# Kernel optimization log

Measured on AMD Instinct MI355X. Metric: run time of the kernel, lower is better.

The kernel has to match this reference:

```python
import jax, jax.numpy as jnp
import numpy as np

T, H, W = 64, 1024, 1024
GRAD_PCT = 0.15
BZ_PCT = 0.3      # 30th percentile of |Bz|


def setup_inputs() -> dict:
    key = jax.random.key(0)
    k1, k2, k3 = jax.random.split(key, 3)
    frames = jax.random.normal(k1, (T, H, W), dtype=jnp.float32)
    observed_mask = jnp.ones((T,), dtype=bool)
    conv_w = jax.random.normal(k2, (4, 1, 3), dtype=jnp.float32) * 0.3  # depthwise OIH
    conv_b = jax.random.normal(k3, (4,), dtype=jnp.float32) * 0.1
    return {"frames": frames, "observed_mask": observed_mask,
            "conv_w": conv_w, "conv_b": conv_b}


def _pil_stats(frames):
    # frames: [T,H,W] -> stats [T,4] (length, intensity, x_centroid, y_centroid)
    T_, H_, W_ = frames.shape
    N = H_ * W_
    gx = jnp.pad(frames[:, :, 1:] - frames[:, :, :-1], ((0, 0), (0, 0), (0, 1)))
    gy = jnp.pad(frames[:, 1:, :] - frames[:, :-1, :], ((0, 0), (0, 1), (0, 0)))
    gm = jnp.sqrt(gx * gx + gy * gy)                    # [T,H,W]
    gm_flat = gm.reshape(T_, N)
    thr = jnp.sort(gm_flat, axis=-1)[:, int((1.0 - GRAD_PCT) * (N - 1))]
    bz_abs = jnp.abs(frames).reshape(T_, N)
    bz_thr = jnp.sort(bz_abs, axis=-1)[:, int(BZ_PCT * (N - 1))]
    mask = ((gm_flat > thr[:, None]) & (bz_abs < bz_thr[:, None])).astype(frames.dtype)
    pil_sum = jnp.clip(mask.sum(-1), 1e-6)
    length = pil_sum / N
    intensity = (gm_flat * mask).sum(-1) / pil_sum
    w3 = (mask * gm_flat).reshape(T_, H_, W_)           # centroid weights
    wsum = jnp.clip(w3.sum((1, 2)), 1e-6)
    xs = jnp.arange(W_, dtype=frames.dtype)
    ys = jnp.arange(H_, dtype=frames.dtype)
    x_cent = jnp.einsum('thw,w->t', w3, xs) / wsum / W_
    y_cent = jnp.einsum('thw,h->t', w3, ys) / wsum / H_
    return jnp.stack([length, intensity, x_cent, y_cent], axis=-1)


def reference(frames, observed_mask, conv_w, conv_b):
    # observed_mask is all-True -> all T frames observed (static n_obs = T)
    n = frames.shape[0]
    stats = _pil_stats(frames)                          # [T,4]
    x = stats.T[None]                                   # [1,4,T]
    y = jax.lax.conv_general_dilated(
        x, conv_w, window_strides=(1,), padding=((1, 1),),
        feature_group_count=4, dimension_numbers=('NCH', 'OIH', 'NCH'))
    s = (y + conv_b[None, :, None])[0].T                # [T,4] smoothed
    length, intensity, x_cent, y_cent = s[:, 0], s[:, 1], s[:, 2], s[:, 3]
    length_mean = length.mean()
    intensity_mean = intensity.mean()
    t_norm = jnp.linspace(0.0, 1.0, n)
    length_trend = ((length - length_mean) * (t_norm - 0.5)).sum() * 6 / n
    intensity_trend = ((intensity - intensity_mean) * (t_norm - 0.5)).sum() * 6 / n
    dx = x_cent[1:] - x_cent[:-1]
    dy = y_cent[1:] - y_cent[:-1]
    speeds = jnp.sqrt(dx * dx + dy * dy)
    motion_speed = speeds.mean()
    motion_direction = jnp.arctan2(dy.sum(), dx.sum()) / np.pi
    growth_rate = (length[-1] - length[0]) / max(1, n - 1)
    instability = jnp.std(speeds, ddof=1)               # unbiased, per-step speeds
    return jnp.stack([length_mean, length_trend, intensity_mean, intensity_trend,
                      motion_speed, motion_direction, growth_rate, instability])
```

## Files before the change

### kernel.cpp

```cpp
#include <hip/hip_runtime.h>
#include <math.h>
#include <stddef.h>

constexpr int T_ = 64;
constexpr int H_ = 1024;
constexpr int W_ = 1024;
constexpr int N_ = H_ * W_;
constexpr unsigned RANK_G = 891288;
constexpr unsigned RANK_B = 314572;

constexpr int ROWS_PER_BLOCK = 32;
constexpr int BLOCKS_PER_FRAME = H_ / ROWS_PER_BLOCK;

constexpr int SROWS = 16;
constexpr int NS = SROWS * W_;
constexpr int SHB = 8192;
constexpr int MARGIN = 192;
constexpr int RS_G = (int)(RANK_G / 64);
constexpr int RS_B = (int)(RANK_B / 64);

constexpr unsigned CAPG = 1536;
constexpr unsigned CAPB = 1536;
constexpr unsigned CAPX = 448;

constexpr unsigned CACHE_N = 26624;
constexpr int SEL_THREADS = 512;

constexpr int RES_SPLIT = 8;

typedef float f4_t __attribute__((ext_vector_type(4)));

struct WS {
  unsigned lo[2][T_], hi[2][T_];
  unsigned cntG[T_][32], cntB[T_][32], cntX[T_][32];
  unsigned cbG[T_][32], cbB[T_][32];
  float    thr[2][T_];
  double   part[T_][32][4];
  double   acc2[T_][RES_SPLIT][4];
  unsigned Gg[T_][32][CAPG];
  unsigned Ga[T_][32][CAPG];
  unsigned Bb[T_][32][CAPB];
  unsigned Xg[T_][32][CAPX];
  unsigned Xb[T_][32][CAPX];
  unsigned Xa[T_][32][CAPX];
};

__device__ __forceinline__ float gm_at(float cur, float right, float down,
                                       int col, int row) {
  float gx = (col < W_ - 1) ? (right - cur) : 0.0f;
  float gy = (row < H_ - 1) ? (down - cur) : 0.0f;
  return sqrtf(gx * gx + gy * gy);
}

template <int NT>
__device__ __forceinline__ unsigned excl_scan_block(unsigned v, int tx,
                                                    volatile unsigned* wsum) {
  const int lane = tx & 63, wv = tx >> 6;
  unsigned s = v;
#pragma unroll
  for (int o = 1; o < 64; o <<= 1) {
    unsigned u = __shfl_up(s, o);
    if (lane >= o) s += u;
  }
  if (lane == 63) wsum[wv] = s;
  __syncthreads();
  unsigned base = 0;
#pragma unroll
  for (int w = 0; w < NT / 64; ++w)
    if (w < wv) base += wsum[w];
  __syncthreads();
  return base + s - v;
}

__global__ __launch_bounds__(256) void sample_kernel(const float* __restrict__ frames,
                                                     WS* ws) {
  const int t = blockIdx.x;
  __shared__ unsigned hist[2][SHB];
  __shared__ unsigned sub[4][1024];
  __shared__ unsigned wscan[4];
  __shared__ unsigned selB[4], selCB[4];
  const int tx = threadIdx.x, c = tx * 4, lane = tx & 63;
  for (int i = tx; i < 2 * SHB; i += 256) (&hist[0][0])[i] = 0;
  for (int i = tx; i < 4 * 1024; i += 256) (&sub[0][0])[i] = 0;
  __syncthreads();
  const float* f = frames + (size_t)t * N_;

#pragma unroll 4
  for (int r = 0; r < SROWS; ++r) {
    const int h = r * 64 + 32;
    const float* row = f + (size_t)h * W_;
    f4_t a = *(const f4_t*)(row + c);
    f4_t b = *(const f4_t*)(row + W_ + c);
    float an = __shfl_down(a.x, 1);
    if (lane == 63) an = (c + 4 < W_) ? row[c + 4] : 0.0f;
    float xs[5] = {a.x, a.y, a.z, a.w, an};
    float ys[4] = {b.x, b.y, b.z, b.w};
#pragma unroll
    for (int j = 0; j < 4; ++j) {
      float gm = gm_at(xs[j], xs[j + 1], ys[j], c + j, h);
      float bz = fabsf(xs[j]);
      atomicAdd(&hist[0][__float_as_uint(gm) >> 18], 1u);
      atomicAdd(&hist[1][__float_as_uint(bz) >> 18], 1u);
    }
  }
  __syncthreads();

  for (int q = 0; q < 2; ++q) {
    unsigned s = 0;
#pragma unroll
    for (int j = 0; j < SHB / 256; ++j) s += hist[q][tx * (SHB / 256) + j];
    unsigned cb = excl_scan_block<256>(s, tx, wscan);
#pragma unroll
    for (int e = 0; e < 2; ++e) {
      int k = (q == 0 ? RS_G : RS_B) + (e == 0 ? -MARGIN : MARGIN);
      if ((unsigned)k >= cb && (unsigned)k < cb + s) {
        unsigned rem = (unsigned)k - cb, cum = 0;
        for (int j = 0; j < SHB / 256; ++j) {
          unsigned hv = hist[q][tx * (SHB / 256) + j];
          if (rem < cum + hv) {
            selB[q * 2 + e]  = tx * (SHB / 256) + j;
            selCB[q * 2 + e] = cb + cum;
            break;
          }
          cum += hv;
        }
      }
    }
    __syncthreads();
  }

#pragma unroll 4
  for (int r = 0; r < SROWS; ++r) {
    const int h = r * 64 + 32;
    const float* row = f + (size_t)h * W_;
    f4_t a = *(const f4_t*)(row + c);
    f4_t b = *(const f4_t*)(row + W_ + c);
    float an = __shfl_down(a.x, 1);
    if (lane == 63) an = (c + 4 < W_) ? row[c + 4] : 0.0f;
    float xs[5] = {a.x, a.y, a.z, a.w, an};
    float ys[4] = {b.x, b.y, b.z, b.w};
#pragma unroll
    for (int j = 0; j < 4; ++j) {
      float gm = gm_at(xs[j], xs[j + 1], ys[j], c + j, h);
      float bz = fabsf(xs[j]);
      unsigned ug = __float_as_uint(gm), ub = __float_as_uint(bz);
#pragma unroll
      for (int e = 0; e < 2; ++e) {
        if ((ug >> 18) == selB[e])     atomicAdd(&sub[e][(ug >> 8) & 1023u], 1u);
        if ((ub >> 18) == selB[2 + e]) atomicAdd(&sub[2 + e][(ub >> 8) & 1023u], 1u);
      }
    }
  }
  __syncthreads();

  for (int qe = 0; qe < 4; ++qe) {
    unsigned s = 0;
#pragma unroll
    for (int j = 0; j < 4; ++j) s += sub[qe][tx * 4 + j];
    unsigned cb = excl_scan_block<256>(s, tx, wscan);
    int q = qe >> 1, e = qe & 1;
    int k0 = (q == 0 ? RS_G : RS_B) + (e == 0 ? -MARGIN : MARGIN);
    unsigned k = (unsigned)k0 - selCB[qe];
    if (k >= cb && k < cb + s) {
      unsigned rem = k - cb, cum = 0;
      for (int j = 0; j < 4; ++j) {
        unsigned hv = sub[qe][tx * 4 + j];
        if (rem < cum + hv) {
          unsigned sb = tx * 4 + j;
          unsigned bound = (selB[qe] << 18) | (sb << 8);
          if (e == 0) ws->lo[q][t] = bound;
          else        ws->hi[q][t] = bound + 256u;
          break;
        }
        cum += hv;
      }
    }
    __syncthreads();
  }
}

__global__ __launch_bounds__(256) void main_kernel(const float* __restrict__ frames,
                                                   WS* ws) {
  const int t = blockIdx.y, blk = blockIdx.x, r0 = blk * ROWS_PER_BLOCK;
  const unsigned lg = ws->lo[0][t], hg = ws->hi[0][t];
  const unsigned lb = ws->lo[1][t], hb = ws->hi[1][t];
  __shared__ unsigned cnt[3];
  const int tx = threadIdx.x, c = tx * 4, lane = tx & 63, wave = tx >> 6;
  if (tx < 3) cnt[tx] = 0;
  __syncthreads();
  unsigned* __restrict__ Gg = ws->Gg[t][blk];
  unsigned* __restrict__ Ga = ws->Ga[t][blk];
  unsigned* __restrict__ Bb = ws->Bb[t][blk];
  unsigned* __restrict__ Xg = ws->Xg[t][blk];
  unsigned* __restrict__ Xb = ws->Xb[t][blk];
  unsigned* __restrict__ Xa = ws->Xa[t][blk];
  const float* f = frames + (size_t)t * N_;

  unsigned cbg = 0, cbb = 0;
  float s0 = 0.f, s1 = 0.f, s2 = 0.f, s3 = 0.f;

  const float* row0 = f + (size_t)r0 * W_;
  f4_t a = __builtin_nontemporal_load((const f4_t*)(row0 + c));
  float an = __shfl_down(a.x, 1);
  if (lane == 63) an = (c + 4 < W_) ? row0[c + 4] : 0.0f;

#pragma unroll 2
  for (int r = 0; r < ROWS_PER_BLOCK; ++r) {
    const int h = r0 + r;
    f4_t b; float bn;
    if (h + 1 < H_) {
      const float* rowN = f + (size_t)(h + 1) * W_;
      b  = __builtin_nontemporal_load((const f4_t*)(rowN + c));
      bn = __shfl_down(b.x, 1);
      if (lane == 63) bn = (c + 4 < W_) ? rowN[c + 4] : 0.0f;
    } else {
      b = a; bn = an;
    }
    float xs[5] = {a.x, a.y, a.z, a.w, an};
    float ys[4] = {b.x, b.y, b.z, b.w};
#pragma unroll
    for (int j = 0; j < 4; ++j) {
      float gm = gm_at(xs[j], xs[j + 1], ys[j], c + j, h);
      float bz = fabsf(xs[j]);
      unsigned ug = __float_as_uint(gm);
      unsigned ub = __float_as_uint(bz);
      bool bz_lo = (ub < lb);
      if (ug < lg) {
        cbg++;
      } else if (ug < hg) {
        unsigned o = atomicAdd(&cnt[0], 1u);
        if (o < CAPG) {
          Gg[o] = ug;
          Ga[o] = (unsigned)(c + j) | ((unsigned)h << 10) | (bz_lo ? (1u << 20) : 0u);
        }
      }
      if (bz_lo) {
        cbb++;
        if (ug >= hg) {
          s0 += 1.0f; s1 += gm;
          s2 += gm * (float)(c + j); s3 += gm * (float)h;
        }
      } else if (ub < hb) {
        unsigned o = atomicAdd(&cnt[1], 1u);
        if (o < CAPB) Bb[o] = ub;
        if (ug >= lg) {
          unsigned o2 = atomicAdd(&cnt[2], 1u);
          if (o2 < CAPX) {
            Xg[o2] = ug; Xb[o2] = ub;
            Xa[o2] = (unsigned)(c + j) | ((unsigned)h << 10);
          }
        }
      }
    }
    a = b; an = bn;
  }

  for (int off = 32; off; off >>= 1) {
    cbg += __shfl_down(cbg, off);
    cbb += __shfl_down(cbb, off);
    s0  += __shfl_down(s0, off);
    s1  += __shfl_down(s1, off);
    s2  += __shfl_down(s2, off);
    s3  += __shfl_down(s3, off);
  }
  __shared__ unsigned wcb[2][4];
  __shared__ float wss[4][4];
  if (lane == 0) {
    wcb[0][wave] = cbg; wcb[1][wave] = cbb;
    wss[0][wave] = s0; wss[1][wave] = s1; wss[2][wave] = s2; wss[3][wave] = s3;
  }
  __syncthreads();
  if (tx == 0) {
    ws->cbG[t][blk] = wcb[0][0] + wcb[0][1] + wcb[0][2] + wcb[0][3];
    ws->cbB[t][blk] = wcb[1][0] + wcb[1][1] + wcb[1][2] + wcb[1][3];
    ws->part[t][blk][0] = (double)wss[0][0] + wss[0][1] + wss[0][2] + wss[0][3];
    ws->part[t][blk][1] = (double)wss[1][0] + wss[1][1] + wss[1][2] + wss[1][3];
    ws->part[t][blk][2] = (double)wss[2][0] + wss[2][1] + wss[2][2] + wss[2][3];
    ws->part[t][blk][3] = (double)wss[3][0] + wss[3][1] + wss[3][2] + wss[3][3];
    ws->cntG[t][blk] = min(cnt[0], CAPG);
    ws->cntB[t][blk] = min(cnt[1], CAPB);
    ws->cntX[t][blk] = min(cnt[2], CAPX);
  }
}

__global__ __launch_bounds__(SEL_THREADS) void select_kernel(WS* ws) {
  const int t = blockIdx.x, q = blockIdx.y, tx = threadIdx.x;
  __shared__ unsigned cache[CACHE_N];
  __shared__ unsigned hist[2048];
  __shared__ unsigned wscan[SEL_THREADS / 64];
  __shared__ unsigned nseg[32], segbase[33];
  __shared__ unsigned sel[2];
  __shared__ unsigned shrank;
  const unsigned lo = ws->lo[q][t];
  const unsigned hi = ws->hi[q][t];
  if (tx < 32) nseg[tx] = (q == 0) ? ws->cntG[t][tx] : ws->cntB[t][tx];
  __syncthreads();
  if (tx == 0) {
    unsigned cb = 0, base = 0;
    for (int i = 0; i < 32; ++i) {
      segbase[i] = base; base += nseg[i];
      cb += (q == 0) ? ws->cbG[t][i] : ws->cbB[t][i];
    }
    segbase[32] = base;
    long long rk = (long long)((q == 0) ? RANK_G : RANK_B) - (long long)cb;
    if (rk < 0) rk = 0;
    if (base > 0 && rk >= (long long)base) rk = (long long)base - 1;
    shrank = (unsigned)rk;
  }
  __syncthreads();
  const unsigned total = segbase[32];
  if (total == 0) {
    if (tx == 0) ws->thr[q][t] = __uint_as_float(lo);
    return;
  }
  const unsigned range = hi - lo;
  const int w = 32 - __clz(range | 1u);
  int sp = (w > 11) ? (w - 11) : 0;
  unsigned rank = shrank, base_val = 0;
  unsigned flt_span = 0xFFFFFFFFu;
  bool first = true;

  while (true) {
    for (int i = tx; i < 2048; i += SEL_THREADS) hist[i] = 0;
    __syncthreads();

    if (first) {
      for (int blk = 0; blk < 32; ++blk) {
        const unsigned n = nseg[blk], sb = segbase[blk];
        const unsigned* __restrict__ ptr = (q == 0) ? ws->Gg[t][blk] : ws->Bb[t][blk];
        for (unsigned i = tx; i < n; i += SEL_THREADS) {
          unsigned d = ptr[i] - lo;
          unsigned slot = sb + i;
          if (slot < CACHE_N) cache[slot] = d;
          atomicAdd(&hist[d >> sp], 1u);
        }
      }
    } else {
      const unsigned lim = (total < CACHE_N) ? total : CACHE_N;
      for (unsigned i = tx; i < lim; i += SEL_THREADS) {
        unsigned rel = cache[i] - base_val;
        if (rel < flt_span) atomicAdd(&hist[rel >> sp], 1u);
      }
      if (total > CACHE_N) {
        for (int blk = 0; blk < 32; ++blk) {
          const unsigned sb = segbase[blk], n = nseg[blk];
          if (sb + n <= CACHE_N) continue;
          const unsigned start = (sb < CACHE_N) ? (CACHE_N - sb) : 0;
          const unsigned* __restrict__ ptr = (q == 0) ? ws->Gg[t][blk] : ws->Bb[t][blk];
          for (unsigned i = start + tx; i < n; i += SEL_THREADS) {
            unsigned rel = (ptr[i] - lo) - base_val;
            if (rel < flt_span) atomicAdd(&hist[rel >> sp], 1u);
          }
        }
      }
    }
    __syncthreads();

    unsigned s = 0;
#pragma unroll
    for (int j = 0; j < 2048 / SEL_THREADS; ++j) s += hist[tx * (2048 / SEL_THREADS) + j];
    unsigned cb2 = excl_scan_block<SEL_THREADS>(s, tx, wscan);
    if (rank >= cb2 && rank < cb2 + s) {
      unsigned rem = rank - cb2, cum = 0;
#pragma unroll
      for (int j = 0; j < 2048 / SEL_THREADS; ++j) {
        unsigned hv = hist[tx * (2048 / SEL_THREADS) + j];
        if (rem < cum + hv) { sel[0] = tx * (2048 / SEL_THREADS) + j; sel[1] = rem - cum; break; }
        cum += hv;
      }
    }
    __syncthreads();
    rank = sel[1];
    base_val += sel[0] << sp;
    if (sp == 0) {
      if (tx == 0) ws->thr[q][t] = __uint_as_float(lo + base_val);
      break;
    }
    flt_span = 1u << sp;
    sp = (sp > 11) ? (sp - 11) : 0;
    first = false;
    __syncthreads();
  }
}

__global__ __launch_bounds__(256) void resolve_kernel(WS* ws) {
  const int t = blockIdx.x, p = blockIdx.y, tx = threadIdx.x;
  const unsigned tg = __float_as_uint(ws->thr[0][t]);
  const unsigned tb = __float_as_uint(ws->thr[1][t]);
  float c = 0.f, sg = 0.f, sx = 0.f, sy = 0.f;
  for (int blk = p * 4; blk < p * 4 + 4; ++blk) {
    const unsigned nG = ws->cntG[t][blk];
    const unsigned* __restrict__ Gg = ws->Gg[t][blk];
    const unsigned* __restrict__ Ga = ws->Ga[t][blk];
    for (unsigned i = tx; i < nG; i += 256) {
      unsigned g = Gg[i], a = Ga[i];
      if (g > tg && (a & (1u << 20))) {
        float v = __uint_as_float(g);
        c += 1.f; sg += v;
        sx += v * (float)(a & 1023u);
        sy += v * (float)((a >> 10) & 1023u);
      }
    }
    const unsigned nX = ws->cntX[t][blk];
    const unsigned* __restrict__ Xg = ws->Xg[t][blk];
    const unsigned* __restrict__ Xb = ws->Xb[t][blk];
    const unsigned* __restrict__ Xa = ws->Xa[t][blk];
    for (unsigned i = tx; i < nX; i += 256) {
      unsigned g = Xg[i], bb = Xb[i], a = Xa[i];
      if (g > tg && bb < tb) {
        float v = __uint_as_float(g);
        c += 1.f; sg += v;
        sx += v * (float)(a & 1023u);
        sy += v * (float)((a >> 10) & 1023u);
      }
    }
  }
  double dc = c, dg = sg, dx = sx, dy = sy;
  if (tx < 4) {
    const double* pp = ws->part[t][p * 4 + tx];
    dc += pp[0]; dg += pp[1]; dx += pp[2]; dy += pp[3];
  }
  for (int off = 32; off; off >>= 1) {
    dc += __shfl_down(dc, off);
    dg += __shfl_down(dg, off);
    dx += __shfl_down(dx, off);
    dy += __shfl_down(dy, off);
  }
  __shared__ double pd[4][4];
  const int wave = tx >> 6, lane = tx & 63;
  if (lane == 0) { pd[0][wave] = dc; pd[1][wave] = dg; pd[2][wave] = dx; pd[3][wave] = dy; }
  __syncthreads();
  if (tx == 0) {
    ws->acc2[t][p][0] = pd[0][0] + pd[0][1] + pd[0][2] + pd[0][3];
    ws->acc2[t][p][1] = pd[1][0] + pd[1][1] + pd[1][2] + pd[1][3];
    ws->acc2[t][p][2] = pd[2][0] + pd[2][1] + pd[2][2] + pd[2][3];
    ws->acc2[t][p][3] = pd[3][0] + pd[3][1] + pd[3][2] + pd[3][3];
  }
}

__global__ __launch_bounds__(64) void finalize_kernel(WS* ws,
                                                      const float* __restrict__ conv_w,
                                                      const float* __restrict__ conv_b,
                                                      float* __restrict__ out) {
  __shared__ float st[T_][4];
  __shared__ float s[T_][4];
  const int tx = threadIdx.x;
  if (tx < T_) {
    double cnt = 0.0, sgm = 0.0, swx = 0.0, swy = 0.0;
#pragma unroll
    for (int b = 0; b < RES_SPLIT; ++b) {
      cnt += ws->acc2[tx][b][0];
      sgm += ws->acc2[tx][b][1];
      swx += ws->acc2[tx][b][2];
      swy += ws->acc2[tx][b][3];
    }
    float pil  = fmaxf((float)cnt, 1e-6f);
    float wsum = fmaxf((float)sgm, 1e-6f);
    st[tx][0] = pil / (float)N_;
    st[tx][1] = (float)sgm / pil;
    st[tx][2] = (float)swx / wsum / (float)W_;
    st[tx][3] = (float)swy / wsum / (float)H_;
  }
  __syncthreads();
  if (tx < T_) {
#pragma unroll
    for (int c2 = 0; c2 < 4; ++c2) {
      float acc = conv_b[c2];
#pragma unroll
      for (int k = 0; k < 3; ++k) {
        int ti = tx + k - 1;
        if (ti >= 0 && ti < T_) acc += conv_w[c2 * 3 + k] * st[ti][c2];
      }
      s[tx][c2] = acc;
    }
  }
  __syncthreads();
  if (tx == 0) {
    float lm = 0.f, im = 0.f;
    for (int i = 0; i < T_; ++i) { lm += s[i][0]; im += s[i][1]; }
    lm /= (float)T_; im /= (float)T_;
    float lt = 0.f, it = 0.f;
    for (int i = 0; i < T_; ++i) {
      float tn = (float)i / (float)(T_ - 1) - 0.5f;
      lt += (s[i][0] - lm) * tn;
      it += (s[i][1] - im) * tn;
    }
    lt *= 6.0f / (float)T_;
    it *= 6.0f / (float)T_;
    float speeds[T_ - 1];
    float spsum = 0.f, sdx = 0.f, sdy = 0.f;
    for (int i = 0; i < T_ - 1; ++i) {
      float dx = s[i + 1][2] - s[i][2];
      float dy = s[i + 1][3] - s[i][3];
      float sp = sqrtf(dx * dx + dy * dy);
      speeds[i] = sp; spsum += sp; sdx += dx; sdy += dy;
    }
    float ms  = spsum / (float)(T_ - 1);
    float dir = atan2f(sdy, sdx) / 3.14159265358979323846f;
    float gr  = (s[T_ - 1][0] - s[0][0]) / (float)(T_ - 1);
    float var = 0.f;
    for (int i = 0; i < T_ - 1; ++i) { float d = speeds[i] - ms; var += d * d; }
    float inst = sqrtf(var / (float)(T_ - 2));
    out[0] = lm; out[1] = lt; out[2] = im; out[3] = it;
    out[4] = ms; out[5] = dir; out[6] = gr; out[7] = inst;
  }
}

extern "C" void kernel_launch(void* const* d_in, const int* in_sizes, int n_in,
                              void* d_out, int out_size, void* d_ws, size_t ws_size,
                              hipStream_t stream) {
  const float* frames = (const float*)d_in[0];
  const float* conv_w = (const float*)d_in[2];
  const float* conv_b = (const float*)d_in[3];
  float* out = (float*)d_out;
  WS* ws = (WS*)d_ws;


  sample_kernel<<<T_, 256, 0, stream>>>(frames, ws);
  main_kernel<<<dim3(BLOCKS_PER_FRAME, T_), 256, 0, stream>>>(frames, ws);
  select_kernel<<<dim3(T_, 2), SEL_THREADS, 0, stream>>>(ws);
  resolve_kernel<<<dim3(T_, RES_SPLIT), 256, 0, stream>>>(ws);
  finalize_kernel<<<1, 64, 0, stream>>>(ws, conv_w, conv_b, out);
}
```

Measured before the change: 502.7 us.

## Fuse select, resolve and finalize kernels using last-block-done atomics

Merges the threshold selection, the resolve pass and the finalize step into one kernel. Per-frame atomic counters pick the second-finishing block to run the resolve for that frame, and a global counter picks the last block to compute the final outputs. The aim is to drop two kernel launches and their inter-kernel gaps. In exchange, resolve now runs on only 64 blocks instead of 512, so that pass has less parallelism, and correctness depends on release/acquire ordering and on the counters being reset in sample_kernel.

```diff
diff --git a/kernel.cpp b/kernel.cpp
--- a/kernel.cpp
+++ b/kernel.cpp
@@ -26,17 +26,18 @@
 constexpr unsigned CACHE_N = 26624;
 constexpr int SEL_THREADS = 512;
 
-constexpr int RES_SPLIT = 8;
-
 typedef float f4_t __attribute__((ext_vector_type(4)));
 
 struct WS {
   unsigned lo[2][T_], hi[2][T_];
   unsigned cntG[T_][32], cntB[T_][32], cntX[T_][32];
   unsigned cbG[T_][32], cbB[T_][32];
-  float    thr[2][T_];
+  unsigned thrb[2][T_];
+  unsigned done[T_];
+  unsigned ndone;
+  unsigned pad_[63];
   double   part[T_][32][4];
-  double   acc2[T_][RES_SPLIT][4];
+  unsigned long long accb[T_][4];
   unsigned Gg[T_][32][CAPG];
   unsigned Ga[T_][32][CAPG];
   unsigned Bb[T_][32][CAPB];
@@ -80,6 +81,7 @@
   __shared__ unsigned wscan[4];
   __shared__ unsigned selB[4], selCB[4];
   const int tx = threadIdx.x, c = tx * 4, lane = tx & 63;
+  if (tx == 0) { ws->done[t] = 0; if (t == 0) ws->ndone = 0; }
   for (int i = tx; i < 2 * SHB; i += 256) (&hist[0][0])[i] = 0;
   for (int i = tx; i < 4 * 1024; i += 256) (&sub[0][0])[i] = 0;
   __syncthreads();
@@ -283,7 +285,9 @@
   }
 }
 
-__global__ __launch_bounds__(SEL_THREADS) void select_kernel(WS* ws) {
+__global__ __launch_bounds__(SEL_THREADS) void fused_kernel(WS* ws,
+    const float* __restrict__ conv_w, const float* __restrict__ conv_b,
+    float* __restrict__ out) {
   const int t = blockIdx.x, q = blockIdx.y, tx = threadIdx.x;
   __shared__ unsigned cache[CACHE_N];
   __shared__ unsigned hist[2048];
@@ -291,6 +295,7 @@
   __shared__ unsigned nseg[32], segbase[33];
   __shared__ unsigned sel[2];
   __shared__ unsigned shrank;
+  __shared__ unsigned role;
   const unsigned lo = ws->lo[q][t];
   const unsigned hi = ws->hi[q][t];
   if (tx < 32) nseg[tx] = (q == 0) ? ws->cntG[t][tx] : ws->cntB[t][tx];
@@ -309,90 +314,95 @@
   }
   __syncthreads();
   const unsigned total = segbase[32];
-  if (total == 0) {
-    if (tx == 0) ws->thr[q][t] = __uint_as_float(lo);
-    return;
-  }
-  const unsigned range = hi - lo;
-  const int w = 32 - __clz(range | 1u);
-  int sp = (w > 11) ? (w - 11) : 0;
-  unsigned rank = shrank, base_val = 0;
-  unsigned flt_span = 0xFFFFFFFFu;
-  bool first = true;
-
-  while (true) {
-    for (int i = tx; i < 2048; i += SEL_THREADS) hist[i] = 0;
-    __syncthreads();
-
-    if (first) {
-      for (int blk = 0; blk < 32; ++blk) {
-        const unsigned n = nseg[blk], sb = segbase[blk];
-        const unsigned* __restrict__ ptr = (q == 0) ? ws->Gg[t][blk] : ws->Bb[t][blk];
-        for (unsigned i = tx; i < n; i += SEL_THREADS) {
-          unsigned d = ptr[i] - lo;
-          unsigned slot = sb + i;
-          if (slot < CACHE_N) cache[slot] = d;
-          atomicAdd(&hist[d >> sp], 1u);
-        }
-      }
-    } else {
-      const unsigned lim = (total < CACHE_N) ? total : CACHE_N;
-      for (unsigned i = tx; i < lim; i += SEL_THREADS) {
-        unsigned rel = cache[i] - base_val;
-        if (rel < flt_span) atomicAdd(&hist[rel >> sp], 1u);
-      }
-      if (total > CACHE_N) {
+  unsigned thr_bits = lo;
+
+  if (total > 0) {
+    const unsigned range = hi - lo;
+    const int w = 32 - __clz(range | 1u);
+    int sp = (w > 11) ? (w - 11) : 0;
+    unsigned rank = shrank, base_val = 0;
+    unsigned flt_span = 0xFFFFFFFFu;
+    bool first = true;
+
+    while (true) {
+      for (int i = tx; i < 2048; i += SEL_THREADS) hist[i] = 0;
+      __syncthreads();
+
+      if (first) {
         for (int blk = 0; blk < 32; ++blk) {
-          const unsigned sb = segbase[blk], n = nseg[blk];
-          if (sb + n <= CACHE_N) continue;
-          const unsigned start = (sb < CACHE_N) ? (CACHE_N - sb) : 0;
+          const unsigned n = nseg[blk], sb = segbase[blk];
           const unsigned* __restrict__ ptr = (q == 0) ? ws->Gg[t][blk] : ws->Bb[t][blk];
-          for (unsigned i = start + tx; i < n; i += SEL_THREADS) {
-            unsigned rel = (ptr[i] - lo) - base_val;
-            if (rel < flt_span) atomicAdd(&hist[rel >> sp], 1u);
+          for (unsigned i = tx; i < n; i += SEL_THREADS) {
+            unsigned d = ptr[i] - lo;
+            unsigned slot = sb + i;
+            if (slot < CACHE_N) cache[slot] = d;
+            atomicAdd(&hist[d >> sp], 1u);
           }
         }
-      }
-    }
-    __syncthreads();
-
-    unsigned s = 0;
-#pragma unroll
-    for (int j = 0; j < 2048 / SEL_THREADS; ++j) s += hist[tx * (2048 / SEL_THREADS) + j];
-    unsigned cb2 = excl_scan_block<SEL_THREADS>(s, tx, wscan);
-    if (rank >= cb2 && rank < cb2 + s) {
-      unsigned rem = rank - cb2, cum = 0;
-#pragma unroll
-      for (int j = 0; j < 2048 / SEL_THREADS; ++j) {
-        unsigned hv = hist[tx * (2048 / SEL_THREADS) + j];
-        if (rem < cum + hv) { sel[0] = tx * (2048 / SEL_THREADS) + j; sel[1] = rem - cum; break; }
-        cum += hv;
-      }
-    }
-    __syncthreads();
-    rank = sel[1];
-    base_val += sel[0] << sp;
-    if (sp == 0) {
-      if (tx == 0) ws->thr[q][t] = __uint_as_float(lo + base_val);
-      break;
-    }
-    flt_span = 1u << sp;
-    sp = (sp > 11) ? (sp - 11) : 0;
-    first = false;
-    __syncthreads();
-  }
-}
-
-__global__ __launch_bounds__(256) void resolve_kernel(WS* ws) {
-  const int t = blockIdx.x, p = blockIdx.y, tx = threadIdx.x;
-  const unsigned tg = __float_as_uint(ws->thr[0][t]);
-  const unsigned tb = __float_as_uint(ws->thr[1][t]);
+      } else {
+        const unsigned lim = (total < CACHE_N) ? total : CACHE_N;
+        for (unsigned i = tx; i < lim; i += SEL_THREADS) {
+          unsigned rel = cache[i] - base_val;
+          if (rel < flt_span) atomicAdd(&hist[rel >> sp], 1u);
+        }
+        if (total > CACHE_N) {
+          for (int blk = 0; blk < 32; ++blk) {
+            const unsigned sb = segbase[blk], n = nseg[blk];
+            if (sb + n <= CACHE_N) continue;
+            const unsigned start = (sb < CACHE_N) ? (CACHE_N - sb) : 0;
+            const unsigned* __restrict__ ptr = (q == 0) ? ws->Gg[t][blk] : ws->Bb[t][blk];
+            for (unsigned i = start + tx; i < n; i += SEL_THREADS) {
+              unsigned rel = (ptr[i] - lo) - base_val;
+              if (rel < flt_span) atomicAdd(&hist[rel >> sp], 1u);
+            }
+          }
+        }
+      }
+      __syncthreads();
+
+      unsigned s = 0;
+#pragma unroll
+      for (int j = 0; j < 2048 / SEL_THREADS; ++j) s += hist[tx * (2048 / SEL_THREADS) + j];
+      unsigned cb2 = excl_scan_block<SEL_THREADS>(s, tx, wscan);
+      if (rank >= cb2 && rank < cb2 + s) {
+        unsigned rem = rank - cb2, cum = 0;
+#pragma unroll
+        for (int j = 0; j < 2048 / SEL_THREADS; ++j) {
+          unsigned hv = hist[tx * (2048 / SEL_THREADS) + j];
+          if (rem < cum + hv) { sel[0] = tx * (2048 / SEL_THREADS) + j; sel[1] = rem - cum; break; }
+          cum += hv;
+        }
+      }
+      __syncthreads();
+      rank = sel[1];
+      base_val += sel[0] << sp;
+      if (sp == 0) { thr_bits = lo + base_val; break; }
+      flt_span = 1u << sp;
+      sp = (sp > 11) ? (sp - 11) : 0;
+      first = false;
+      __syncthreads();
+    }
+  }
+
+  if (tx == 0) {
+    __hip_atomic_store(&ws->thrb[q][t], thr_bits, __ATOMIC_RELEASE,
+                       __HIP_MEMORY_SCOPE_AGENT);
+    role = __hip_atomic_fetch_add(&ws->done[t], 1u, __ATOMIC_ACQ_REL,
+                                  __HIP_MEMORY_SCOPE_AGENT);
+  }
+  __syncthreads();
+  if (role == 0) return;
+
+  const unsigned tg = __hip_atomic_load(&ws->thrb[0][t], __ATOMIC_ACQUIRE,
+                                        __HIP_MEMORY_SCOPE_AGENT);
+  const unsigned tb = __hip_atomic_load(&ws->thrb[1][t], __ATOMIC_ACQUIRE,
+                                        __HIP_MEMORY_SCOPE_AGENT);
   float c = 0.f, sg = 0.f, sx = 0.f, sy = 0.f;
-  for (int blk = p * 4; blk < p * 4 + 4; ++blk) {
+  for (int blk = 0; blk < 32; ++blk) {
     const unsigned nG = ws->cntG[t][blk];
     const unsigned* __restrict__ Gg = ws->Gg[t][blk];
     const unsigned* __restrict__ Ga = ws->Ga[t][blk];
-    for (unsigned i = tx; i < nG; i += 256) {
+    for (unsigned i = tx; i < nG; i += SEL_THREADS) {
       unsigned g = Gg[i], a = Ga[i];
       if (g > tg && (a & (1u << 20))) {
         float v = __uint_as_float(g);
@@ -405,7 +415,7 @@
     const unsigned* __restrict__ Xg = ws->Xg[t][blk];
     const unsigned* __restrict__ Xb = ws->Xb[t][blk];
     const unsigned* __restrict__ Xa = ws->Xa[t][blk];
-    for (unsigned i = tx; i < nX; i += 256) {
+    for (unsigned i = tx; i < nX; i += SEL_THREADS) {
       unsigned g = Xg[i], bb = Xb[i], a = Xa[i];
       if (g > tg && bb < tb) {
         float v = __uint_as_float(g);
@@ -416,8 +426,8 @@
     }
   }
   double dc = c, dg = sg, dx = sx, dy = sy;
-  if (tx < 4) {
-    const double* pp = ws->part[t][p * 4 + tx];
+  if (tx < 32) {
+    const double* pp = ws->part[t][tx];
     dc += pp[0]; dg += pp[1]; dx += pp[2]; dy += pp[3];
   }
   for (int off = 32; off; off >>= 1) {
@@ -426,34 +436,41 @@
     dx += __shfl_down(dx, off);
     dy += __shfl_down(dy, off);
   }
-  __shared__ double pd[4][4];
+  __shared__ double pd[4][SEL_THREADS / 64];
   const int wave = tx >> 6, lane = tx & 63;
   if (lane == 0) { pd[0][wave] = dc; pd[1][wave] = dg; pd[2][wave] = dx; pd[3][wave] = dy; }
   __syncthreads();
   if (tx == 0) {
-    ws->acc2[t][p][0] = pd[0][0] + pd[0][1] + pd[0][2] + pd[0][3];
-    ws->acc2[t][p][1] = pd[1][0] + pd[1][1] + pd[1][2] + pd[1][3];
-    ws->acc2[t][p][2] = pd[2][0] + pd[2][1] + pd[2][2] + pd[2][3];
-    ws->acc2[t][p][3] = pd[3][0] + pd[3][1] + pd[3][2] + pd[3][3];
-  }
-}
-
-__global__ __launch_bounds__(64) void finalize_kernel(WS* ws,
-                                                      const float* __restrict__ conv_w,
-                                                      const float* __restrict__ conv_b,
-                                                      float* __restrict__ out) {
+    double a0 = 0, a1 = 0, a2 = 0, a3 = 0;
+#pragma unroll
+    for (int w = 0; w < SEL_THREADS / 64; ++w) {
+      a0 += pd[0][w]; a1 += pd[1][w]; a2 += pd[2][w]; a3 += pd[3][w];
+    }
+    __hip_atomic_store(&ws->accb[t][0], (unsigned long long)__double_as_longlong(a0),
+                       __ATOMIC_RELAXED, __HIP_MEMORY_SCOPE_AGENT);
+    __hip_atomic_store(&ws->accb[t][1], (unsigned long long)__double_as_longlong(a1),
+                       __ATOMIC_RELAXED, __HIP_MEMORY_SCOPE_AGENT);
+    __hip_atomic_store(&ws->accb[t][2], (unsigned long long)__double_as_longlong(a2),
+                       __ATOMIC_RELAXED, __HIP_MEMORY_SCOPE_AGENT);
+    __hip_atomic_store(&ws->accb[t][3], (unsigned long long)__double_as_longlong(a3),
+                       __ATOMIC_RELAXED, __HIP_MEMORY_SCOPE_AGENT);
+    role = __hip_atomic_fetch_add(&ws->ndone, 1u, __ATOMIC_ACQ_REL,
+                                  __HIP_MEMORY_SCOPE_AGENT);
+  }
+  __syncthreads();
+  if (role != (unsigned)(T_ - 1)) return;
+
   __shared__ float st[T_][4];
-  __shared__ float s[T_][4];
-  const int tx = threadIdx.x;
+  __shared__ float sA[T_][4];
   if (tx < T_) {
-    double cnt = 0.0, sgm = 0.0, swx = 0.0, swy = 0.0;
-#pragma unroll
-    for (int b = 0; b < RES_SPLIT; ++b) {
-      cnt += ws->acc2[tx][b][0];
-      sgm += ws->acc2[tx][b][1];
-      swx += ws->acc2[tx][b][2];
-      swy += ws->acc2[tx][b][3];
-    }
+    double cnt = __longlong_as_double((long long)__hip_atomic_load(
+        &ws->accb[tx][0], __ATOMIC_ACQUIRE, __HIP_MEMORY_SCOPE_AGENT));
+    double sgm = __longlong_as_double((long long)__hip_atomic_load(
+        &ws->accb[tx][1], __ATOMIC_ACQUIRE, __HIP_MEMORY_SCOPE_AGENT));
+    double swx = __longlong_as_double((long long)__hip_atomic_load(
+        &ws->accb[tx][2], __ATOMIC_ACQUIRE, __HIP_MEMORY_SCOPE_AGENT));
+    double swy = __longlong_as_double((long long)__hip_atomic_load(
+        &ws->accb[tx][3], __ATOMIC_ACQUIRE, __HIP_MEMORY_SCOPE_AGENT));
     float pil  = fmaxf((float)cnt, 1e-6f);
     float wsum = fmaxf((float)sgm, 1e-6f);
     st[tx][0] = pil / (float)N_;
@@ -471,33 +488,33 @@
         int ti = tx + k - 1;
         if (ti >= 0 && ti < T_) acc += conv_w[c2 * 3 + k] * st[ti][c2];
       }
-      s[tx][c2] = acc;
+      sA[tx][c2] = acc;
     }
   }
   __syncthreads();
   if (tx == 0) {
     float lm = 0.f, im = 0.f;
-    for (int i = 0; i < T_; ++i) { lm += s[i][0]; im += s[i][1]; }
+    for (int i = 0; i < T_; ++i) { lm += sA[i][0]; im += sA[i][1]; }
     lm /= (float)T_; im /= (float)T_;
     float lt = 0.f, it = 0.f;
     for (int i = 0; i < T_; ++i) {
       float tn = (float)i / (float)(T_ - 1) - 0.5f;
-      lt += (s[i][0] - lm) * tn;
-      it += (s[i][1] - im) * tn;
+      lt += (sA[i][0] - lm) * tn;
+      it += (sA[i][1] - im) * tn;
     }
     lt *= 6.0f / (float)T_;
     it *= 6.0f / (float)T_;
     float speeds[T_ - 1];
     float spsum = 0.f, sdx = 0.f, sdy = 0.f;
     for (int i = 0; i < T_ - 1; ++i) {
-      float dx = s[i + 1][2] - s[i][2];
-      float dy = s[i + 1][3] - s[i][3];
-      float sp = sqrtf(dx * dx + dy * dy);
-      speeds[i] = sp; spsum += sp; sdx += dx; sdy += dy;
+      float dxv = sA[i + 1][2] - sA[i][2];
+      float dyv = sA[i + 1][3] - sA[i][3];
+      float sp = sqrtf(dxv * dxv + dyv * dyv);
+      speeds[i] = sp; spsum += sp; sdx += dxv; sdy += dyv;
     }
     float ms  = spsum / (float)(T_ - 1);
     float dir = atan2f(sdy, sdx) / 3.14159265358979323846f;
-    float gr  = (s[T_ - 1][0] - s[0][0]) / (float)(T_ - 1);
+    float gr  = (sA[T_ - 1][0] - sA[0][0]) / (float)(T_ - 1);
     float var = 0.f;
     for (int i = 0; i < T_ - 1; ++i) { float d = speeds[i] - ms; var += d * d; }
     float inst = sqrtf(var / (float)(T_ - 2));
@@ -518,7 +535,5 @@
 
   sample_kernel<<<T_, 256, 0, stream>>>(frames, ws);
   main_kernel<<<dim3(BLOCKS_PER_FRAME, T_), 256, 0, stream>>>(frames, ws);
-  select_kernel<<<dim3(T_, 2), SEL_THREADS, 0, stream>>>(ws);
-  resolve_kernel<<<dim3(T_, RES_SPLIT), 256, 0, stream>>>(ws);
-  finalize_kernel<<<1, 64, 0, stream>>>(ws, conv_w, conv_b, out);
+  fused_kernel<<<dim3(T_, 2), SEL_THREADS, 0, stream>>>(ws, conv_w, conv_b, out);
 }
```

New measurement: 562.5 us. +11.9%, slower.
